# Kernel tuning notes

Measured on AMD Instinct MI355X. Metric: run time of the kernel, lower is better.

## Reference

```python
import jax, jax.numpy as jnp
import numpy as np

N_NEIGHBORS = 9
MIN_STD, MAX_STD = 0.01, 0.5
EPS = 1e-8


def setup_inputs() -> dict:
    key = jax.random.key(0)
    k1, k2, k3 = jax.random.split(key, 3)
    B, C, H, W = 8, 2048, 28, 28
    M = 8192
    features = jax.random.normal(k1, (B, C, H, W), dtype=jnp.float32)
    memory_bank = jax.random.normal(k2, (M, C), dtype=jnp.float32)
    influence_weight = jnp.ones((C,), dtype=jnp.float32)
    distance_weight = jnp.ones((1,), dtype=jnp.float32)
    noise_unit = jax.random.normal(k3, (B * H * W, C), dtype=jnp.float32)
    return {
        "features": features,
        "memory_bank": memory_bank,
        "influence_weight": influence_weight,
        "distance_weight": distance_weight,
        "noise_unit": noise_unit,
    }


def _std(x, axis=None, keepdims=False):
    # torch.std default: unbiased (ddof=1)
    return jnp.std(x, axis=axis, keepdims=keepdims, ddof=1)


def reference(features, memory_bank, influence_weight, distance_weight, noise_unit):
    B, C, H, W = features.shape
    M = memory_bank.shape[0]
    k = min(N_NEIGHBORS, M)

    # [B*H*W, C]
    f = features.transpose(0, 2, 3, 1).reshape(B * H * W, C)

    # Euclidean cdist via the (||a||^2 + ||b||^2 - 2 a.b) expansion
    f2 = jnp.sum(f * f, axis=1, keepdims=True)            # [N,1]
    m2 = jnp.sum(memory_bank * memory_bank, axis=1)       # [M]
    d2 = f2 + m2[None, :] - 2.0 * (f @ memory_bank.T)     # [N,M]
    dist = jnp.sqrt(jnp.clip(d2, 0.0, None))

    # top-k smallest distances (sorted ascending, like torch.topk largest=False)
    neg_vals, idx = jax.lax.top_k(-dist, k)               # [N,k]
    topk_distances = -neg_vals

    # gather neighbor features and per-dim influence
    nn_feats = memory_bank[idx]                           # [N,k,C]
    influence_scores = jnp.mean(jnp.abs(f[:, None, :] - nn_feats), axis=1)  # [N,C]
    influence_scores = influence_scores * influence_weight[None, :]

    # normalize influence per-row
    influence_norm = influence_scores - jnp.mean(influence_scores, axis=-1, keepdims=True)
    influence_norm = influence_norm / (_std(influence_scores, axis=-1, keepdims=True) + EPS)

    # distance signal: row-mean distance, broadcast to [N,C], global-normalized
    ds = jnp.mean(topk_distances, axis=-1, keepdims=True)  # [N,1]
    ds_e = jnp.broadcast_to(ds, influence_norm.shape)      # [N,C]
    distance_norm = (ds_e - jnp.mean(ds_e)) / (_std(ds_e) + EPS)

    combined = influence_norm + distance_weight * distance_norm
    noise_std = MIN_STD + (MAX_STD - MIN_STD) * jax.nn.sigmoid(combined)  # [N,C]

    noised_flat = f + noise_unit * noise_std
    noised_features = noised_flat.reshape(B, H, W, C).transpose(0, 3, 1, 2)
    influence_map = jnp.mean(influence_scores, axis=-1).reshape(B, H, W)
    noise_std_map = jnp.mean(noise_std, axis=-1).reshape(B, H, W)
    return noised_features, influence_map, noise_std_map
```

## Files before the change

### kernel.cpp

```cpp
#include <hip/hip_runtime.h>
#include <math.h>

typedef __attribute__((ext_vector_type(8))) __bf16 bf16x8;
typedef __attribute__((ext_vector_type(4))) float f32x4;

#define NB 8
#define NC 2048
#define NHW 784
#define NROWS 6272
#define NM 8192
#define NNEI 9
#define NCAND 16
#define NKT 64

static_assert(NROWS == NB * NHW, "dims");

__device__ __forceinline__ unsigned umin32(unsigned a, unsigned b) { return a < b ? a : b; }

__global__ __launch_bounds__(256) void prep_f_kernel(const float* __restrict__ feat,
                                                     float* __restrict__ Af32,
                                                     __bf16* __restrict__ Ahi) {
  __shared__ float tile[32][33];
  int b = blockIdx.z;
  int c0 = blockIdx.y * 32;
  int hw0 = blockIdx.x * 32;
  int tx = threadIdx.x & 31, ty = threadIdx.x >> 5;
#pragma unroll
  for (int i = 0; i < 4; ++i) {
    int c = c0 + ty + i * 8;
    int hw = hw0 + tx;
    float v = 0.f;
    if (hw < NHW) v = feat[((size_t)b * NC + c) * NHW + hw];
    tile[ty + i * 8][tx] = v;
  }
  __syncthreads();
#pragma unroll
  for (int i = 0; i < 4; ++i) {
    int hwl = ty + i * 8;
    int hw = hw0 + hwl;
    if (hw < NHW) {
      int n = b * NHW + hw;
      float v = tile[tx][hwl];
      Af32[(size_t)n * NC + c0 + tx] = v;
      Ahi[(size_t)n * NC + c0 + tx] = (__bf16)v;
    }
  }
}

__global__ __launch_bounds__(256) void prep_mb_kernel(const float* __restrict__ mb,
                                                      __bf16* __restrict__ Bhi,
                                                      float* __restrict__ m2) {
  __shared__ float red[4];
  int m = blockIdx.x, tid = threadIdx.x;
  float ss = 0.f;
#pragma unroll
  for (int i = 0; i < NC / 256; ++i) {
    int c = tid + i * 256;
    float v = mb[(size_t)m * NC + c];
    Bhi[(size_t)m * NC + c] = (__bf16)v;
    ss += v * v;
  }
#pragma unroll
  for (int off = 32; off; off >>= 1) ss += __shfl_xor(ss, off);
  if ((tid & 63) == 0) red[tid >> 6] = ss;
  __syncthreads();
  if (tid == 0) m2[m] = red[0] + red[1] + red[2] + red[3];
}

#define STAGE(SRC, DST) \
  __builtin_amdgcn_global_load_lds((const __attribute__((address_space(1))) void*)(SRC), \
                                   (__attribute__((address_space(3))) void*)(DST), 16, 0, 0)

__global__ __launch_bounds__(512, 2) void gemm8_kernel(const __bf16* __restrict__ Ahi,
                                                       const __bf16* __restrict__ Bhi,
                                                       const float* __restrict__ m2,
                                                       unsigned short* __restrict__ dotq) {
  __shared__ __align__(16) char lds[131072];
  int tid = threadIdx.x;
  int lane = tid & 63, w = tid >> 6;
  int bid = blockIdx.x;
  int r = lane & 15, kq = lane >> 4;
  int r4 = (lane >> 4) * 4, cL = lane & 15;

  if (bid >= 768) {
    int lb = bid - 768;
    size_t m0l = (size_t)(bid & 7) * 1024 + (size_t)(lb >> 3) * 64;
    int n0l = 6144 + w * 16;
    const __bf16* aB = Ahi + (size_t)(n0l + r) * NC + kq * 8;
    const __bf16* bB[4];
#pragma unroll
    for (int g = 0; g < 4; ++g) bB[g] = Bhi + (m0l + g * 16 + r) * NC + kq * 8;
    f32x4 accl[4] = {};
#pragma unroll 4
    for (int kt = 0; kt < NKT; ++kt) {
      bf16x8 av = *(const bf16x8*)(aB + kt * 32);
#pragma unroll
      for (int g = 0; g < 4; ++g) {
        bf16x8 bvg = *(const bf16x8*)(bB[g] + kt * 32);
        accl[g] = __builtin_amdgcn_mfma_f32_16x16x32_bf16(av, bvg, accl[g], 0, 0, 0);
      }
    }
#pragma unroll
    for (int g = 0; g < 4; ++g) {
      float m2g = m2[m0l + g * 16 + cL];
#pragma unroll
      for (int q = 0; q < 4; ++q) {
        int grow = n0l + r4 + q;
        float sc = m2g - 2.f * accl[g][q];
        int qi = (int)(sc * 16.f);
        qi = qi < 0 ? 0 : (qi > 65535 ? 65535 : qi);
        dotq[(size_t)grow * NM + (m0l + g * 16 + cL)] = (unsigned short)qi;
      }
    }
    return;
  }

  int xcd = bid & 7, lin = bid >> 3;
  int mt = xcd * 4 + (lin & 3), rtl = lin >> 2;
  size_t n0 = (size_t)rtl * 256, m0 = (size_t)mt * 256;
  int wr = w >> 2, wc = w & 3;

  int p = lane & 3;
  const char* aSrc[2];
  const char* bSrc[2];
  int aDst[2], bDst[2];
#pragma unroll
  for (int j = 0; j < 2; ++j) {
    int rloc = (w * 2 + j) * 16 + (lane >> 2);
    int kqs = (p - (rloc >> 1)) & 3;
    aSrc[j] = (const char*)Ahi + (n0 + rloc) * (NC * 2) + kqs * 16;
    bSrc[j] = (const char*)Bhi + (m0 + rloc) * (NC * 2) + kqs * 16;
    aDst[j] = (w * 2 + j) * 1024;
    bDst[j] = 16384 + (w * 2 + j) * 1024;
  }
  int s16 = (kq + (r >> 1)) & 3;
  int aRd = wr * 8192 + r * 64 + s16 * 16;
  int bRd = 16384 + wc * 4096 + r * 64 + s16 * 16;

  f32x4 acc[8][4] = {};

#pragma unroll
  for (int t = 0; t < 2; ++t) {
    int sb = t * 32768, kb = t * 64;
#pragma unroll
    for (int j = 0; j < 2; ++j)
      STAGE(aSrc[j] + kb, lds + sb + aDst[j]);
#pragma unroll
    for (int j = 0; j < 2; ++j)
      STAGE(bSrc[j] + kb, lds + sb + bDst[j]);
  }
  asm volatile("s_waitcnt vmcnt(4)" ::: "memory");
  __builtin_amdgcn_s_barrier();
  __builtin_amdgcn_sched_barrier(0);

#pragma unroll 4
  for (int kt = 0; kt < NKT; ++kt) {
    int sb = (kt & 3) * 32768;
    int kt2 = (kt + 2) & 63;
    int sb2 = (kt2 & 3) * 32768;
    int kb2 = kt2 * 64;
    bf16x8 av[4], bv[4];
#pragma unroll
    for (int j = 0; j < 2; ++j)
      STAGE(aSrc[j] + kb2, lds + sb2 + aDst[j]);
#pragma unroll
    for (int f = 0; f < 4; ++f) av[f] = *(const bf16x8*)(lds + sb + aRd + f * 1024);
#pragma unroll
    for (int g = 0; g < 4; ++g) bv[g] = *(const bf16x8*)(lds + sb + bRd + g * 1024);
    __builtin_amdgcn_s_setprio(1);
#pragma unroll
    for (int f = 0; f < 4; ++f)
#pragma unroll
      for (int g = 0; g < 4; ++g)
        acc[f][g] = __builtin_amdgcn_mfma_f32_16x16x32_bf16(av[f], bv[g], acc[f][g], 0, 0, 0);
    __builtin_amdgcn_s_setprio(0);
#pragma unroll
    for (int j = 0; j < 2; ++j)
      STAGE(bSrc[j] + kb2, lds + sb2 + bDst[j]);
#pragma unroll
    for (int f = 0; f < 4; ++f) av[f] = *(const bf16x8*)(lds + sb + aRd + (f + 4) * 1024);
    __builtin_amdgcn_s_setprio(1);
#pragma unroll
    for (int f = 0; f < 4; ++f)
#pragma unroll
      for (int g = 0; g < 4; ++g)
        acc[f + 4][g] = __builtin_amdgcn_mfma_f32_16x16x32_bf16(av[f], bv[g], acc[f + 4][g], 0, 0, 0);
    __builtin_amdgcn_s_setprio(0);
    asm volatile("s_waitcnt vmcnt(4)" ::: "memory");
    __builtin_amdgcn_s_barrier();
    __builtin_amdgcn_sched_barrier(0);
  }

  float m2r[4];
#pragma unroll
  for (int g = 0; g < 4; ++g) m2r[g] = m2[m0 + wc * 64 + g * 16 + cL];
#pragma unroll
  for (int f = 0; f < 8; ++f) {
    int grow0 = (int)n0 + wr * 128 + f * 16 + r4;
#pragma unroll
    for (int g = 0; g < 4; ++g) {
      size_t gcol = m0 + wc * 64 + g * 16 + cL;
#pragma unroll
      for (int q = 0; q < 4; ++q) {
        float sc = m2r[g] - 2.f * acc[f][g][q];
        int qi = (int)(sc * 16.f);
        qi = qi < 0 ? 0 : (qi > 65535 ? 65535 : qi);
        dotq[(size_t)(grow0 + q) * NM + gcol] = (unsigned short)qi;
      }
    }
  }
}

__global__ __launch_bounds__(256) void selres_kernel(const unsigned short* __restrict__ dotq,
                                                     const float* __restrict__ Af32,
                                                     const float* __restrict__ mb,
                                                     int* __restrict__ tki,
                                                     float* __restrict__ dsv) {
  __shared__ float fbuf[NC];
  __shared__ unsigned wmin[4];
  __shared__ int cidxL[NCAND];
  __shared__ double d2s[NCAND];
  int n = blockIdx.x;
  int tid = threadIdx.x;
  int lane = tid & 63, w = tid >> 6;

  unsigned kk[32];
  {
    const uint4* dq = (const uint4*)(dotq + (size_t)n * NM + tid * 32);
    unsigned base = tid * 32;
#pragma unroll
    for (int s = 0; s < 4; ++s) {
      uint4 v = dq[s];
      unsigned c0 = v.x, c1 = v.y, c2 = v.z, c3 = v.w;
      kk[s * 8 + 0] = ((c0 & 0xFFFFu) << 13) | (base + s * 8 + 0);
      kk[s * 8 + 1] = ((c0 >> 16) << 13)     | (base + s * 8 + 1);
      kk[s * 8 + 2] = ((c1 & 0xFFFFu) << 13) | (base + s * 8 + 2);
      kk[s * 8 + 3] = ((c1 >> 16) << 13)     | (base + s * 8 + 3);
      kk[s * 8 + 4] = ((c2 & 0xFFFFu) << 13) | (base + s * 8 + 4);
      kk[s * 8 + 5] = ((c2 >> 16) << 13)     | (base + s * 8 + 5);
      kk[s * 8 + 6] = ((c3 & 0xFFFFu) << 13) | (base + s * 8 + 6);
      kk[s * 8 + 7] = ((c3 >> 16) << 13)     | (base + s * 8 + 7);
    }
  }
#pragma unroll
  for (int i = 0; i < NC / 256; ++i)
    fbuf[tid + i * 256] = Af32[(size_t)n * NC + tid + i * 256];

  unsigned lmin = 0xFFFFFFFFu;
#pragma unroll
  for (int i = 0; i < 32; ++i) lmin = umin32(lmin, kk[i]);
  unsigned t = lmin;
#pragma unroll
  for (int off = 32; off; off >>= 1) t = umin32(t, (unsigned)__shfl_xor((int)t, off));
  if (lane == 0) wmin[w] = t;
  __syncthreads();

  for (int r = 0; r < NCAND; ++r) {
    unsigned g = umin32(umin32(wmin[0], wmin[1]), umin32(wmin[2], wmin[3]));
    if (tid == 0) cidxL[r] = (int)(g & 8191u);
    __syncthreads();
    int owner = (int)((g & 8191u) >> 5);
    if ((owner >> 6) == w) {
      if (tid == owner) {
#pragma unroll
        for (int i = 0; i < 32; ++i)
          if (kk[i] == g) kk[i] = 0xFFFFFFFFu;
        lmin = 0xFFFFFFFFu;
#pragma unroll
        for (int i = 0; i < 32; ++i) lmin = umin32(lmin, kk[i]);
      }
      unsigned t2 = lmin;
#pragma unroll
      for (int off = 32; off; off >>= 1) t2 = umin32(t2, (unsigned)__shfl_xor((int)t2, off));
      if (lane == 0) wmin[w] = t2;
    }
    __syncthreads();
  }

#pragma unroll
  for (int jj = 0; jj < 4; ++jj) {
    int j = w * 4 + jj;
    const float* mrow = mb + (size_t)cidxL[j] * NC;
    double acc = 0.0;
#pragma unroll
    for (int i = 0; i < 32; ++i) {
      int c = lane + i * 64;
      double d = (double)fbuf[c] - (double)mrow[c];
      acc += d * d;
    }
#pragma unroll
    for (int off = 32; off; off >>= 1) acc += __shfl_xor(acc, off);
    if (lane == 0) d2s[j] = acc;
  }
  __syncthreads();

  if (tid == 0) {
    double dacc = 0.0;
    bool used[NCAND] = {};
    for (int r = 0; r < NNEI; ++r) {
      int bj = 0; double bv = 1e300; int bidx = 0x7fffffff;
      for (int j = 0; j < NCAND; ++j) {
        if (used[j]) continue;
        if (d2s[j] < bv || (d2s[j] == bv && cidxL[j] < bidx)) { bv = d2s[j]; bidx = cidxL[j]; bj = j; }
      }
      used[bj] = true;
      tki[(size_t)n * NNEI + r] = bidx;
      dacc += sqrt(bv > 0.0 ? bv : 0.0);
    }
    dsv[n] = (float)(dacc * (1.0 / 9.0));
  }
}

__global__ __launch_bounds__(256) void stats_kernel(const float* __restrict__ dsv,
                                                    float* __restrict__ stats) {
  __shared__ float buf[NROWS];
  __shared__ float red[4];
  int tid = threadIdx.x;
  float s = 0.f;
  for (int i = tid; i < NROWS; i += 256) { float v = dsv[i]; buf[i] = v; s += v; }
#pragma unroll
  for (int off = 32; off; off >>= 1) s += __shfl_xor(s, off);
  if ((tid & 63) == 0) red[tid >> 6] = s;
  __syncthreads();
  float mu = (red[0] + red[1] + red[2] + red[3]) * (1.f / NROWS);
  __syncthreads();
  float q = 0.f;
  for (int i = tid; i < NROWS; i += 256) { float d = buf[i] - mu; q += d * d; }
#pragma unroll
  for (int off = 32; off; off >>= 1) q += __shfl_xor(q, off);
  if ((tid & 63) == 0) red[tid >> 6] = q;
  __syncthreads();
  if (tid == 0) {
    float SSb = (red[0] + red[1] + red[2] + red[3]) * (float)NC;
    float var = SSb / ((float)NROWS * (float)NC - 1.f);
    stats[0] = mu;
    stats[1] = 1.f / (sqrtf(var) + 1e-8f);
  }
}

__global__ __launch_bounds__(256) void fuse_kernel(const float* __restrict__ Af32,
                                                   const float* __restrict__ mb,
                                                   const float* __restrict__ noise,
                                                   const float* __restrict__ iw,
                                                   const float* __restrict__ dwp,
                                                   const int* __restrict__ topk_idx,
                                                   const float* __restrict__ dsv,
                                                   const float* __restrict__ stats,
                                                   float* __restrict__ noised_tmp,
                                                   float* __restrict__ out_infl,
                                                   float* __restrict__ out_nstd) {
  __shared__ int idx[NNEI];
  __shared__ float red[4];
  int n = blockIdx.x;
  int tid = threadIdx.x;
  if (tid < NNEI) idx[tid] = topk_idx[(size_t)n * NNEI + tid];
  __syncthreads();

  int c0 = tid * 8;
  const float* frow = Af32 + (size_t)n * NC + c0;
  float4 fa = *(const float4*)frow;
  float4 fb = *(const float4*)(frow + 4);
  float f_c[8] = {fa.x, fa.y, fa.z, fa.w, fb.x, fb.y, fb.z, fb.w};
  float a_c[8] = {};
  for (int j = 0; j < NNEI; ++j) {
    const float* mrow = mb + (size_t)idx[j] * NC + c0;
    float4 ma = *(const float4*)mrow;
    float4 mb2 = *(const float4*)(mrow + 4);
    float mv[8] = {ma.x, ma.y, ma.z, ma.w, mb2.x, mb2.y, mb2.z, mb2.w};
#pragma unroll
    for (int k = 0; k < 8; ++k) a_c[k] += fabsf(f_c[k] - mv[k]);
  }
  float4 w0 = *(const float4*)(iw + c0);
  float4 w1 = *(const float4*)(iw + c0 + 4);
  float wv[8] = {w0.x, w0.y, w0.z, w0.w, w1.x, w1.y, w1.z, w1.w};
  float s_c[8];
  float sum_s = 0.f, sum_s2 = 0.f;
#pragma unroll
  for (int k = 0; k < 8; ++k) {
    float s = (a_c[k] * (1.f / 9.f)) * wv[k];
    s_c[k] = s;
    sum_s += s;
    sum_s2 += s * s;
  }
#pragma unroll
  for (int off = 32; off; off >>= 1) sum_s += __shfl_xor(sum_s, off);
  if ((tid & 63) == 0) red[tid >> 6] = sum_s;
  __syncthreads();
  float tot_s = red[0] + red[1] + red[2] + red[3];
  __syncthreads();
#pragma unroll
  for (int off = 32; off; off >>= 1) sum_s2 += __shfl_xor(sum_s2, off);
  if ((tid & 63) == 0) red[tid >> 6] = sum_s2;
  __syncthreads();
  float tot_s2 = red[0] + red[1] + red[2] + red[3];
  __syncthreads();

  float mu = tot_s * (1.f / NC);
  float var = (tot_s2 - (float)NC * mu * mu) * (1.f / (NC - 1));
  float rstd = 1.f / (sqrtf(fmaxf(var, 0.f)) + 1e-8f);
  float dnorm = (dsv[n] - stats[0]) * stats[1];
  float dwv = dwp[0];

  float4 na = *(const float4*)(noise + (size_t)n * NC + c0);
  float4 nb = *(const float4*)(noise + (size_t)n * NC + c0 + 4);
  float nz[8] = {na.x, na.y, na.z, na.w, nb.x, nb.y, nb.z, nb.w};
  float o[8];
  float nsum = 0.f;
#pragma unroll
  for (int k = 0; k < 8; ++k) {
    float inorm = (s_c[k] - mu) * rstd;
    float comb = inorm + dwv * dnorm;
    float sig = 1.f / (1.f + expf(-comb));
    float nstd = 0.01f + 0.49f * sig;
    nsum += nstd;
    o[k] = f_c[k] + nz[k] * nstd;
  }
  float* orow = noised_tmp + (size_t)n * NC + c0;
  *(float4*)orow = make_float4(o[0], o[1], o[2], o[3]);
  *(float4*)(orow + 4) = make_float4(o[4], o[5], o[6], o[7]);
#pragma unroll
  for (int off = 32; off; off >>= 1) nsum += __shfl_xor(nsum, off);
  if ((tid & 63) == 0) red[tid >> 6] = nsum;
  __syncthreads();
  if (tid == 0) {
    out_infl[n] = tot_s * (1.f / NC);
    out_nstd[n] = (red[0] + red[1] + red[2] + red[3]) * (1.f / NC);
  }
}

__global__ __launch_bounds__(256) void transpose_kernel(const float* __restrict__ src,
                                                        float* __restrict__ dst) {
  __shared__ float tile[32][33];
  int b = blockIdx.z;
  int c0 = blockIdx.y * 32;
  int hw0 = blockIdx.x * 32;
  int tx = threadIdx.x & 31, ty = threadIdx.x >> 5;
#pragma unroll
  for (int i = 0; i < 4; ++i) {
    int hw = hw0 + ty + i * 8;
    if (hw < NHW) tile[ty + i * 8][tx] = src[((size_t)(b * NHW + hw)) * NC + c0 + tx];
  }
  __syncthreads();
#pragma unroll
  for (int i = 0; i < 4; ++i) {
    int c = c0 + ty + i * 8;
    int hw = hw0 + tx;
    if (hw < NHW) dst[((size_t)b * NC + c) * NHW + hw] = tile[tx][ty + i * 8];
  }
}

extern "C" void kernel_launch(void* const* d_in, const int* in_sizes, int n_in,
                              void* d_out, int out_size, void* d_ws, size_t ws_size,
                              hipStream_t stream) {
  (void)in_sizes; (void)n_in; (void)out_size; (void)ws_size;
  const float* feat  = (const float*)d_in[0];
  const float* mb    = (const float*)d_in[1];
  const float* iw    = (const float*)d_in[2];
  const float* dwp   = (const float*)d_in[3];
  const float* noise = (const float*)d_in[4];
  float* out = (float*)d_out;
  float* out_noised = out;
  float* out_infl = out + (size_t)NB * NC * NHW;
  float* out_nstd = out_infl + NROWS;

  char* ws = (char*)d_ws;
  size_t off = 0;
  auto alloc = [&](size_t sz) -> char* {
    char* p = ws + off;
    off += (sz + 255) & ~(size_t)255;
    return p;
  };
  float* Af32 = (float*)alloc((size_t)NROWS * NC * 4);
  __bf16* Ahi = (__bf16*)alloc((size_t)NROWS * NC * 2);
  char* region = alloc((size_t)NROWS * NC * 4);
  __bf16* Bhi = (__bf16*)region;
  float* noised_tmp = (float*)region;
  float* m2v = (float*)alloc((size_t)NM * 4);
  int* tki = (int*)alloc((size_t)NROWS * NNEI * 4);
  float* dsv = (float*)alloc((size_t)NROWS * 4);
  float* stv = (float*)alloc(256);
  unsigned short* dotq = (unsigned short*)alloc((size_t)NROWS * NM * 2);

  prep_f_kernel<<<dim3(25, 64, NB), 256, 0, stream>>>(feat, Af32, Ahi);
  prep_mb_kernel<<<NM, 256, 0, stream>>>(mb, Bhi, m2v);
  gemm8_kernel<<<896, 512, 0, stream>>>(Ahi, Bhi, m2v, dotq);
  selres_kernel<<<NROWS, 256, 0, stream>>>(dotq, Af32, mb, tki, dsv);
  stats_kernel<<<1, 256, 0, stream>>>(dsv, stv);
  fuse_kernel<<<NROWS, 256, 0, stream>>>(Af32, mb, noise, iw, dwp, tki, dsv, stv,
                                         noised_tmp, out_infl, out_nstd);
  transpose_kernel<<<dim3(25, 64, NB), 256, 0, stream>>>(noised_tmp, out_noised);
}
```

Baseline: 534.0 us.

## Use 4 waves per GEMM block with 128x128 per-wave tiles and prefetch tail loads

```diff
diff --git a/kernel.cpp b/kernel.cpp
--- a/kernel.cpp
+++ b/kernel.cpp
@@ -71,7 +71,7 @@
   __builtin_amdgcn_global_load_lds((const __attribute__((address_space(1))) void*)(SRC), \
                                    (__attribute__((address_space(3))) void*)(DST), 16, 0, 0)
 
-__global__ __launch_bounds__(512, 2) void gemm8_kernel(const __bf16* __restrict__ Ahi,
+__global__ __launch_bounds__(256, 1) void gemm8_kernel(const __bf16* __restrict__ Ahi,
                                                        const __bf16* __restrict__ Bhi,
                                                        const float* __restrict__ m2,
                                                        unsigned short* __restrict__ dotq) {
@@ -85,31 +85,48 @@
   if (bid >= 768) {
     int lb = bid - 768;
     size_t m0l = (size_t)(bid & 7) * 1024 + (size_t)(lb >> 3) * 64;
-    int n0l = 6144 + w * 16;
-    const __bf16* aB = Ahi + (size_t)(n0l + r) * NC + kq * 8;
+    int n0l = 6144 + w * 32;
+    const __bf16* aB0 = Ahi + (size_t)(n0l + r) * NC + kq * 8;
+    const __bf16* aB1 = aB0 + 16 * NC;
     const __bf16* bB[4];
 #pragma unroll
     for (int g = 0; g < 4; ++g) bB[g] = Bhi + (m0l + g * 16 + r) * NC + kq * 8;
-    f32x4 accl[4] = {};
+    f32x4 accl[2][4] = {};
+    bf16x8 a0 = *(const bf16x8*)aB0, a1 = *(const bf16x8*)aB1;
+    bf16x8 bb0 = *(const bf16x8*)bB[0], bb1 = *(const bf16x8*)bB[1];
+    bf16x8 bb2 = *(const bf16x8*)bB[2], bb3 = *(const bf16x8*)bB[3];
 #pragma unroll 4
     for (int kt = 0; kt < NKT; ++kt) {
-      bf16x8 av = *(const bf16x8*)(aB + kt * 32);
+      int ktn = (kt + 1) & 63;
+      bf16x8 a0n = *(const bf16x8*)(aB0 + ktn * 32);
+      bf16x8 a1n = *(const bf16x8*)(aB1 + ktn * 32);
+      bf16x8 b0n = *(const bf16x8*)(bB[0] + ktn * 32);
+      bf16x8 b1n = *(const bf16x8*)(bB[1] + ktn * 32);
+      bf16x8 b2n = *(const bf16x8*)(bB[2] + ktn * 32);
+      bf16x8 b3n = *(const bf16x8*)(bB[3] + ktn * 32);
+      accl[0][0] = __builtin_amdgcn_mfma_f32_16x16x32_bf16(a0, bb0, accl[0][0], 0, 0, 0);
+      accl[0][1] = __builtin_amdgcn_mfma_f32_16x16x32_bf16(a0, bb1, accl[0][1], 0, 0, 0);
+      accl[0][2] = __builtin_amdgcn_mfma_f32_16x16x32_bf16(a0, bb2, accl[0][2], 0, 0, 0);
+      accl[0][3] = __builtin_amdgcn_mfma_f32_16x16x32_bf16(a0, bb3, accl[0][3], 0, 0, 0);
+      accl[1][0] = __builtin_amdgcn_mfma_f32_16x16x32_bf16(a1, bb0, accl[1][0], 0, 0, 0);
+      accl[1][1] = __builtin_amdgcn_mfma_f32_16x16x32_bf16(a1, bb1, accl[1][1], 0, 0, 0);
+      accl[1][2] = __builtin_amdgcn_mfma_f32_16x16x32_bf16(a1, bb2, accl[1][2], 0, 0, 0);
+      accl[1][3] = __builtin_amdgcn_mfma_f32_16x16x32_bf16(a1, bb3, accl[1][3], 0, 0, 0);
+      a0 = a0n; a1 = a1n; bb0 = b0n; bb1 = b1n; bb2 = b2n; bb3 = b3n;
+    }
+#pragma unroll
+    for (int f = 0; f < 2; ++f) {
+      int grow0 = n0l + f * 16 + r4;
 #pragma unroll
       for (int g = 0; g < 4; ++g) {
-        bf16x8 bvg = *(const bf16x8*)(bB[g] + kt * 32);
-        accl[g] = __builtin_amdgcn_mfma_f32_16x16x32_bf16(av, bvg, accl[g], 0, 0, 0);
-      }
-    }
-#pragma unroll
-    for (int g = 0; g < 4; ++g) {
-      float m2g = m2[m0l + g * 16 + cL];
-#pragma unroll
-      for (int q = 0; q < 4; ++q) {
-        int grow = n0l + r4 + q;
-        float sc = m2g - 2.f * accl[g][q];
-        int qi = (int)(sc * 16.f);
-        qi = qi < 0 ? 0 : (qi > 65535 ? 65535 : qi);
-        dotq[(size_t)grow * NM + (m0l + g * 16 + cL)] = (unsigned short)qi;
+        float m2g = m2[m0l + g * 16 + cL];
+#pragma unroll
+        for (int q = 0; q < 4; ++q) {
+          float sc = m2g - 2.f * accl[f][g][q];
+          int qi = (int)(sc * 16.f);
+          qi = qi < 0 ? 0 : (qi > 65535 ? 65535 : qi);
+          dotq[(size_t)(grow0 + q) * NM + (m0l + g * 16 + cL)] = (unsigned short)qi;
+        }
       }
     }
     return;
@@ -118,88 +135,79 @@
   int xcd = bid & 7, lin = bid >> 3;
   int mt = xcd * 4 + (lin & 3), rtl = lin >> 2;
   size_t n0 = (size_t)rtl * 256, m0 = (size_t)mt * 256;
-  int wr = w >> 2, wc = w & 3;
+  int wr = w >> 1, wc = w & 1;
 
   int p = lane & 3;
-  const char* aSrc[2];
-  const char* bSrc[2];
-  int aDst[2], bDst[2];
-#pragma unroll
-  for (int j = 0; j < 2; ++j) {
-    int rloc = (w * 2 + j) * 16 + (lane >> 2);
+  const char* aSrc[4];
+  const char* bSrc[4];
+  int aDst[4], bDst[4];
+#pragma unroll
+  for (int j = 0; j < 4; ++j) {
+    int rloc = (w * 4 + j) * 16 + (lane >> 2);
     int kqs = (p - (rloc >> 1)) & 3;
     aSrc[j] = (const char*)Ahi + (n0 + rloc) * (NC * 2) + kqs * 16;
     bSrc[j] = (const char*)Bhi + (m0 + rloc) * (NC * 2) + kqs * 16;
-    aDst[j] = (w * 2 + j) * 1024;
-    bDst[j] = 16384 + (w * 2 + j) * 1024;
+    aDst[j] = (w * 4 + j) * 1024;
+    bDst[j] = 16384 + (w * 4 + j) * 1024;
   }
   int s16 = (kq + (r >> 1)) & 3;
   int aRd = wr * 8192 + r * 64 + s16 * 16;
-  int bRd = 16384 + wc * 4096 + r * 64 + s16 * 16;
-
-  f32x4 acc[8][4] = {};
+  int bRd = 16384 + wc * 8192 + r * 64 + s16 * 16;
+
+  f32x4 acc[8][8] = {};
 
 #pragma unroll
   for (int t = 0; t < 2; ++t) {
     int sb = t * 32768, kb = t * 64;
 #pragma unroll
-    for (int j = 0; j < 2; ++j)
+    for (int j = 0; j < 4; ++j)
       STAGE(aSrc[j] + kb, lds + sb + aDst[j]);
 #pragma unroll
-    for (int j = 0; j < 2; ++j)
+    for (int j = 0; j < 4; ++j)
       STAGE(bSrc[j] + kb, lds + sb + bDst[j]);
   }
-  asm volatile("s_waitcnt vmcnt(4)" ::: "memory");
+  asm volatile("s_waitcnt vmcnt(8)" ::: "memory");
   __builtin_amdgcn_s_barrier();
   __builtin_amdgcn_sched_barrier(0);
 
-#pragma unroll 4
+#pragma unroll 2
   for (int kt = 0; kt < NKT; ++kt) {
     int sb = (kt & 3) * 32768;
     int kt2 = (kt + 2) & 63;
     int sb2 = (kt2 & 3) * 32768;
     int kb2 = kt2 * 64;
-    bf16x8 av[4], bv[4];
-#pragma unroll
-    for (int j = 0; j < 2; ++j)
+    bf16x8 av[8], bv[8];
+#pragma unroll
+    for (int j = 0; j < 4; ++j)
       STAGE(aSrc[j] + kb2, lds + sb2 + aDst[j]);
 #pragma unroll
-    for (int f = 0; f < 4; ++f) av[f] = *(const bf16x8*)(lds + sb + aRd + f * 1024);
-#pragma unroll
-    for (int g = 0; g < 4; ++g) bv[g] = *(const bf16x8*)(lds + sb + bRd + g * 1024);
+    for (int f = 0; f < 8; ++f) av[f] = *(const bf16x8*)(lds + sb + aRd + f * 1024);
+#pragma unroll
+    for (int j = 0; j < 4; ++j)
+      STAGE(bSrc[j] + kb2, lds + sb2 + bDst[j]);
+#pragma unroll
+    for (int g = 0; g < 8; ++g) bv[g] = *(const bf16x8*)(lds + sb + bRd + g * 1024);
     __builtin_amdgcn_s_setprio(1);
 #pragma unroll
-    for (int f = 0; f < 4; ++f)
-#pragma unroll
-      for (int g = 0; g < 4; ++g)
+    for (int f = 0; f < 8; ++f)
+#pragma unroll
+      for (int g = 0; g < 8; ++g)
         acc[f][g] = __builtin_amdgcn_mfma_f32_16x16x32_bf16(av[f], bv[g], acc[f][g], 0, 0, 0);
     __builtin_amdgcn_s_setprio(0);
-#pragma unroll
-    for (int j = 0; j < 2; ++j)
-      STAGE(bSrc[j] + kb2, lds + sb2 + bDst[j]);
-#pragma unroll
-    for (int f = 0; f < 4; ++f) av[f] = *(const bf16x8*)(lds + sb + aRd + (f + 4) * 1024);
-    __builtin_amdgcn_s_setprio(1);
-#pragma unroll
-    for (int f = 0; f < 4; ++f)
-#pragma unroll
-      for (int g = 0; g < 4; ++g)
-        acc[f + 4][g] = __builtin_amdgcn_mfma_f32_16x16x32_bf16(av[f], bv[g], acc[f + 4][g], 0, 0, 0);
-    __builtin_amdgcn_s_setprio(0);
-    asm volatile("s_waitcnt vmcnt(4)" ::: "memory");
+    asm volatile("s_waitcnt vmcnt(8)" ::: "memory");
     __builtin_amdgcn_s_barrier();
     __builtin_amdgcn_sched_barrier(0);
   }
 
-  float m2r[4];
-#pragma unroll
-  for (int g = 0; g < 4; ++g) m2r[g] = m2[m0 + wc * 64 + g * 16 + cL];
+  float m2r[8];
+#pragma unroll
+  for (int g = 0; g < 8; ++g) m2r[g] = m2[m0 + wc * 128 + g * 16 + cL];
 #pragma unroll
   for (int f = 0; f < 8; ++f) {
     int grow0 = (int)n0 + wr * 128 + f * 16 + r4;
 #pragma unroll
-    for (int g = 0; g < 4; ++g) {
-      size_t gcol = m0 + wc * 64 + g * 16 + cL;
+    for (int g = 0; g < 8; ++g) {
+      size_t gcol = m0 + wc * 128 + g * 16 + cL;
 #pragma unroll
       for (int q = 0; q < 4; ++q) {
         float sc = m2r[g] - 2.f * acc[f][g][q];
@@ -483,7 +491,7 @@
 
   prep_f_kernel<<<dim3(25, 64, NB), 256, 0, stream>>>(feat, Af32, Ahi);
   prep_mb_kernel<<<NM, 256, 0, stream>>>(mb, Bhi, m2v);
-  gemm8_kernel<<<896, 512, 0, stream>>>(Ahi, Bhi, m2v, dotq);
+  gemm8_kernel<<<896, 256, 0, stream>>>(Ahi, Bhi, m2v, dotq);
   selres_kernel<<<NROWS, 256, 0, stream>>>(dotq, Af32, mb, tki, dsv);
   stats_kernel<<<1, 256, 0, stream>>>(dsv, stv);
   fuse_kernel<<<NROWS, 256, 0, stream>>>(Af32, mb, noise, iw, dwp, tki, dsv, stv,
```

Measured after the change: 630.2 us. +18.0%, slower.
